# Kernel optimization log

Measured on AMD Instinct MI355X. Metric: run time of the kernel, lower is better.

The kernel has to match this reference:

```python
import jax, jax.numpy as jnp
import numpy as np
import math

G = 256        # graphs per batch
N = 2048       # nodes per graph (uniform)
D = 128        # dim_in
E = 4194304    # edges (avg degree 8)
DE = 16        # edge_attr dim
RATIO = 0.5    # cfg.gnn.pool_ratio


def setup_inputs() -> dict:
    key = jax.random.key(0)
    k1, k2, k3, k4 = jax.random.split(key, 4)
    x = jax.random.normal(k1, (G * N, D), jnp.float32)
    edge_index = jax.random.randint(k2, (2, E), 0, G * N, jnp.int32)
    edge_attr = jax.random.normal(k3, (E, DE), jnp.float32)
    batch = jnp.repeat(jnp.arange(G, dtype=jnp.int32), N)
    weight = jax.random.normal(k4, (D,), jnp.float32)  # TopKPooling score projection
    return {"x": x, "edge_index": edge_index, "edge_attr": edge_attr,
            "batch": batch, "weight": weight, "num_graphs": G}


def reference(x, edge_index, edge_attr, batch, weight, num_graphs):
    n_total = x.shape[0]
    n = n_total // num_graphs              # uniform nodes per graph
    k = int(math.ceil(RATIO * n))          # nodes kept per graph (static)

    # PyG TopKPooling score: tanh((x . w) / ||w||)
    score = jnp.tanh((x @ weight) / jnp.linalg.norm(weight))  # [n_total]

    # per-graph top-k (uniform graph sizes -> reshape + lax.top_k)
    top_idx = jax.lax.top_k(score.reshape(num_graphs, n), k)[1]          # [G, k]
    offs = (jnp.arange(num_graphs, dtype=top_idx.dtype) * n)[:, None]
    perm = (top_idx + offs).reshape(-1)                                  # [G*k] global node ids

    # gate kept node features by their score
    x_out = x[perm] * score[perm][:, None]                               # [G*k, D]
    batch_out = jnp.repeat(jnp.arange(num_graphs, dtype=batch.dtype), k)

    # filter_adj: remap kept nodes to new ids, drop edges touching removed nodes
    new_ids = jnp.arange(perm.shape[0], dtype=jnp.int32)
    node_map = jnp.full((n_total,), -1, jnp.int32).at[perm].set(new_ids)
    ns = node_map[edge_index[0]]
    nd = node_map[edge_index[1]]
    edge_mask = (ns >= 0) & (nd >= 0)                                    # [E]
    edge_index_out = jnp.where(edge_mask, jnp.stack([ns, nd]), -1)       # [2, E], -1 = dropped
    edge_attr_out = jnp.where(edge_mask[:, None], edge_attr, 0.0)        # [E, DE]

    return x_out, edge_index_out, edge_attr_out, batch_out, edge_mask
```

## Files before the change

kernel.cpp:

```cpp
#include <hip/hip_runtime.h>


__global__ void norm_kernel(const float* __restrict__ w,
                            float* __restrict__ inv_norm) {
  int l = threadIdx.x;
  float2 wv = reinterpret_cast<const float2*>(w)[l];
  float s = wv.x * wv.x + wv.y * wv.y;
#pragma unroll
  for (int off = 32; off > 0; off >>= 1) s += __shfl_xor(s, off);
  if (l == 0) *inv_norm = __frsqrt_rn(s);
}

__global__ __launch_bounds__(256) void score_kernel(
    const float* __restrict__ x, const float* __restrict__ w,
    const float* __restrict__ inv_norm, double* __restrict__ keys,
    float* __restrict__ gate, int n_total) {
  int t = (int)(blockIdx.x * 256u + threadIdx.x);
  int row = t >> 4;
  int sub = t & 15;
  if (row >= n_total) return;
  const float4* xp = reinterpret_cast<const float4*>(x + (size_t)row * 128 + sub * 8);
  const float4* wp = reinterpret_cast<const float4*>(w + sub * 8);
  float4 a = xp[0], b = xp[1];
  float4 wa = wp[0], wb = wp[1];
  double dot = (double)a.x * wa.x + (double)a.y * wa.y +
               (double)a.z * wa.z + (double)a.w * wa.w +
               (double)b.x * wb.x + (double)b.y * wb.y +
               (double)b.z * wb.z + (double)b.w * wb.w;
#pragma unroll
  for (int off = 8; off > 0; off >>= 1) dot += __shfl_xor(dot, off);
  if (sub == 0) {
    keys[row] = dot;
    gate[row] = tanhf((float)dot * inv_norm[0]);
  }
}

#define TK_PAD(j) ((j) + ((j) >> 4))
__global__ __launch_bounds__(1024) void topk_kernel(
    const double* __restrict__ keys, int* __restrict__ perm,
    int* __restrict__ node_map, int n, int k) {
  __shared__ unsigned long long skey[2048 + 128];
  __shared__ int sidx[2048 + 128];
  const int g = blockIdx.x;
  const int tid = threadIdx.x;

  for (int j = tid; j < n; j += 1024) {
    unsigned long long b =
        (unsigned long long)__double_as_longlong(keys[(size_t)g * n + j]);
    unsigned long long u = (b & 0x8000000000000000ULL) ? ~b : (b | 0x8000000000000000ULL);
    skey[TK_PAD(j)] = ~u;
    sidx[TK_PAD(j)] = j;
  }

  for (int size = 2; size <= n; size <<= 1) {
    for (int stride = size >> 1; stride > 0; stride >>= 1) {
      __syncthreads();
      int lo = ((tid & ~(stride - 1)) << 1) | (tid & (stride - 1));
      int hi = lo + stride;
      bool asc = ((lo & size) == 0);
      int plo = TK_PAD(lo), phi = TK_PAD(hi);
      unsigned long long ka = skey[plo], kb = skey[phi];
      int ia = sidx[plo], ib = sidx[phi];
      bool hi_lt_lo = (kb < ka) || (kb == ka && ib < ia);
      bool lo_lt_hi = (ka < kb) || (ka == kb && ia < ib);
      if (asc ? hi_lt_lo : lo_lt_hi) {
        skey[plo] = kb; skey[phi] = ka;
        sidx[plo] = ib; sidx[phi] = ia;
      }
    }
  }
  __syncthreads();

  for (int r = tid; r < n; r += 1024) {
    int node = g * n + sidx[TK_PAD(r)];
    node_map[node] = (r < k) ? (g * k + r) : -1;
    if (r < k) perm[g * k + r] = node;
  }
}

__global__ __launch_bounds__(256) void gather_kernel(
    const float* __restrict__ x, const float* __restrict__ gate,
    const int* __restrict__ perm, float* __restrict__ x_out,
    float* __restrict__ batch_out, int total_rows, int k) {
  int t = (int)(blockIdx.x * 256u + threadIdx.x);
  int row = t >> 5;
  int d4 = t & 31;
  if (row >= total_rows) return;
  int src = perm[row];
  float s = gate[src];
  float4 v = *reinterpret_cast<const float4*>(x + (size_t)src * 128 + d4 * 4);
  v.x *= s; v.y *= s; v.z *= s; v.w *= s;
  *reinterpret_cast<float4*>(x_out + (size_t)row * 128 + d4 * 4) = v;
  if (d4 == 0) batch_out[row] = (float)(row / k);
}

__global__ __launch_bounds__(256) void edge_kernel(
    const int* __restrict__ edge_index, const int* __restrict__ node_map,
    const float4* __restrict__ attr, float* __restrict__ eio,
    float* __restrict__ mask_out, float4* __restrict__ attr_out, int E) {
  __shared__ float smask[256];
  const int base = (int)(blockIdx.x * 256u);
  const int e = base + threadIdx.x;
  int ns = node_map[edge_index[e]];
  int nd = node_map[edge_index[E + e]];
  bool m = (ns >= 0) && (nd >= 0);
  float z = m ? 1.0f : 0.0f;
  eio[e] = m ? (float)ns : -1.0f;
  eio[E + e] = m ? (float)nd : -1.0f;
  mask_out[e] = z;
  smask[threadIdx.x] = z;
  __syncthreads();
  const float4* ablk = attr + (size_t)base * 4;
  float4* oblk = attr_out + (size_t)base * 4;
#pragma unroll
  for (int it = 0; it < 4; ++it) {
    int idx = it * 256 + (int)threadIdx.x;
    float zz = smask[idx >> 2];
    float4 a = ablk[idx];
    a.x *= zz; a.y *= zz; a.z *= zz; a.w *= zz;
    oblk[idx] = a;
  }
}

extern "C" void kernel_launch(void* const* d_in, const int* in_sizes, int n_in,
                              void* d_out, int out_size, void* d_ws, size_t ws_size,
                              hipStream_t stream) {
  const float* x          = (const float*)d_in[0];
  const int*   edge_index = (const int*)d_in[1];
  const float* edge_attr  = (const float*)d_in[2];
  const float* w          = (const float*)d_in[4];

  const int D = 128;
  const int n_total = in_sizes[0] / D;
  const int E = in_sizes[1] / 2;
  const int G = 256;
  const int n = n_total / G;
  const int k = (n + 1) / 2;
  const int total_rows = G * k;

  float* out       = (float*)d_out;
  float* x_out     = out;
  float* eio       = x_out + (size_t)total_rows * D;
  float* attr_out  = eio + (size_t)2 * E;
  float* batch_out = attr_out + (size_t)E * 16;
  float* mask_out  = batch_out + total_rows;

  double* keys   = (double*)d_ws;
  float* gate    = (float*)((char*)d_ws + (size_t)n_total * 8);
  int* perm      = (int*)(gate + n_total);
  int* node_map  = perm + total_rows;
  float* inv_nrm = (float*)(node_map + n_total);

  norm_kernel<<<1, 64, 0, stream>>>(w, inv_nrm);
  score_kernel<<<(n_total * 16) / 256, 256, 0, stream>>>(
      x, w, inv_nrm, keys, gate, n_total);
  topk_kernel<<<G, 1024, 0, stream>>>(keys, perm, node_map, n, k);
  gather_kernel<<<(total_rows * 32) / 256, 256, 0, stream>>>(
      x, gate, perm, x_out, batch_out, total_rows, k);
  edge_kernel<<<E / 256, 256, 0, stream>>>(
      edge_index, node_map, (const float4*)edge_attr, eio, mask_out,
      (float4*)attr_out, E);
}
```

Measured before the change: 272.3 us.

## Fuse gather and edge filter into one kernel, drop norm kernel, nontemporal stores

Merges the gather and edge-filter kernels into a single launch whose block index picks which of the two jobs a block does. The norm kernel and the stored gate array are removed: the gate tanh is recomputed in the gather path from the double keys, with the weight norm recomputed per block. Streaming loads and stores now use nontemporal builtins, and each block handles more rows or edges. This saves two launches and the gate traffic, at the cost of redundant per-block norm reductions and a branchy mixed-role kernel.

```diff
diff --git a/kernel.cpp b/kernel.cpp
--- a/kernel.cpp
+++ b/kernel.cpp
@@ -1,20 +1,20 @@
 #include <hip/hip_runtime.h>
 
 
-__global__ void norm_kernel(const float* __restrict__ w,
-                            float* __restrict__ inv_norm) {
-  int l = threadIdx.x;
-  float2 wv = reinterpret_cast<const float2*>(w)[l];
-  float s = wv.x * wv.x + wv.y * wv.y;
-#pragma unroll
-  for (int off = 32; off > 0; off >>= 1) s += __shfl_xor(s, off);
-  if (l == 0) *inv_norm = __frsqrt_rn(s);
+typedef float f32x4_v __attribute__((ext_vector_type(4)));
+
+__device__ inline void nt_store4(float4 v, float4* p) {
+  f32x4_v t; t.x = v.x; t.y = v.y; t.z = v.z; t.w = v.w;
+  __builtin_nontemporal_store(t, reinterpret_cast<f32x4_v*>(p));
+}
+__device__ inline float4 nt_load4(const float4* p) {
+  f32x4_v t = __builtin_nontemporal_load(reinterpret_cast<const f32x4_v*>(p));
+  return make_float4(t.x, t.y, t.z, t.w);
 }
 
 __global__ __launch_bounds__(256) void score_kernel(
     const float* __restrict__ x, const float* __restrict__ w,
-    const float* __restrict__ inv_norm, double* __restrict__ keys,
-    float* __restrict__ gate, int n_total) {
+    double* __restrict__ keys, int n_total) {
   int t = (int)(blockIdx.x * 256u + threadIdx.x);
   int row = t >> 4;
   int sub = t & 15;
@@ -29,10 +29,7 @@
                (double)b.z * wb.z + (double)b.w * wb.w;
 #pragma unroll
   for (int off = 8; off > 0; off >>= 1) dot += __shfl_xor(dot, off);
-  if (sub == 0) {
-    keys[row] = dot;
-    gate[row] = tanhf((float)dot * inv_norm[0]);
-  }
+  if (sub == 0) keys[row] = dot;
 }
 
 #define TK_PAD(j) ((j) + ((j) >> 4))
@@ -78,47 +75,64 @@
   }
 }
 
-__global__ __launch_bounds__(256) void gather_kernel(
-    const float* __restrict__ x, const float* __restrict__ gate,
-    const int* __restrict__ perm, float* __restrict__ x_out,
-    float* __restrict__ batch_out, int total_rows, int k) {
-  int t = (int)(blockIdx.x * 256u + threadIdx.x);
-  int row = t >> 5;
-  int d4 = t & 31;
-  if (row >= total_rows) return;
-  int src = perm[row];
-  float s = gate[src];
-  float4 v = *reinterpret_cast<const float4*>(x + (size_t)src * 128 + d4 * 4);
-  v.x *= s; v.y *= s; v.z *= s; v.w *= s;
-  *reinterpret_cast<float4*>(x_out + (size_t)row * 128 + d4 * 4) = v;
-  if (d4 == 0) batch_out[row] = (float)(row / k);
-}
+__global__ __launch_bounds__(256) void output_kernel(
+    const float* __restrict__ x, const double* __restrict__ keys,
+    const float* __restrict__ w, const int* __restrict__ perm,
+    const int* __restrict__ node_map, const int* __restrict__ edge_index,
+    const float4* __restrict__ attr, float* __restrict__ x_out,
+    float* __restrict__ batch_out, float* __restrict__ eio,
+    float* __restrict__ mask_out, float4* __restrict__ attr_out,
+    int E, int k, int NB_G) {
+  const int bid = (int)blockIdx.x;
+  if (bid < NB_G) {
+    int l = threadIdx.x & 63;
+    float2 wv = reinterpret_cast<const float2*>(w)[l];
+    float wsq = wv.x * wv.x + wv.y * wv.y;
+#pragma unroll
+    for (int off = 32; off > 0; off >>= 1) wsq += __shfl_xor(wsq, off);
+    float inv = __frsqrt_rn(wsq);
 
-__global__ __launch_bounds__(256) void edge_kernel(
-    const int* __restrict__ edge_index, const int* __restrict__ node_map,
-    const float4* __restrict__ attr, float* __restrict__ eio,
-    float* __restrict__ mask_out, float4* __restrict__ attr_out, int E) {
-  __shared__ float smask[256];
-  const int base = (int)(blockIdx.x * 256u);
-  const int e = base + threadIdx.x;
-  int ns = node_map[edge_index[e]];
-  int nd = node_map[edge_index[E + e]];
-  bool m = (ns >= 0) && (nd >= 0);
-  float z = m ? 1.0f : 0.0f;
-  eio[e] = m ? (float)ns : -1.0f;
-  eio[E + e] = m ? (float)nd : -1.0f;
-  mask_out[e] = z;
-  smask[threadIdx.x] = z;
-  __syncthreads();
-  const float4* ablk = attr + (size_t)base * 4;
-  float4* oblk = attr_out + (size_t)base * 4;
+    int d4 = threadIdx.x & 31;
+    int rbase = bid * 32 + ((int)threadIdx.x >> 5);
 #pragma unroll
-  for (int it = 0; it < 4; ++it) {
-    int idx = it * 256 + (int)threadIdx.x;
-    float zz = smask[idx >> 2];
-    float4 a = ablk[idx];
-    a.x *= zz; a.y *= zz; a.z *= zz; a.w *= zz;
-    oblk[idx] = a;
+    for (int r4 = 0; r4 < 4; ++r4) {
+      int row = rbase + r4 * 8;
+      int src = perm[row];
+      float s = tanhf((float)keys[src] * inv);
+      float4 v = *reinterpret_cast<const float4*>(x + (size_t)src * 128 + d4 * 4);
+      v.x *= s; v.y *= s; v.z *= s; v.w *= s;
+      nt_store4(v, reinterpret_cast<float4*>(x_out + (size_t)row * 128 + d4 * 4));
+      if (d4 == 0)
+        __builtin_nontemporal_store((float)(row / k), batch_out + row);
+    }
+  } else {
+    __shared__ float smask[256];
+    const int ebase = (bid - NB_G) * 512;
+    for (int it = 0; it < 2; ++it) {
+      int e = ebase + it * 256 + (int)threadIdx.x;
+      int s0 = __builtin_nontemporal_load(edge_index + e);
+      int s1 = __builtin_nontemporal_load(edge_index + E + e);
+      int ns = node_map[s0];
+      int nd = node_map[s1];
+      bool m = (ns >= 0) && (nd >= 0);
+      float z = m ? 1.0f : 0.0f;
+      __builtin_nontemporal_store(m ? (float)ns : -1.0f, eio + e);
+      __builtin_nontemporal_store(m ? (float)nd : -1.0f, eio + E + e);
+      __builtin_nontemporal_store(z, mask_out + e);
+      smask[threadIdx.x] = z;
+      __syncthreads();
+      const float4* ablk = attr + (size_t)(ebase + it * 256) * 4;
+      float4* oblk = attr_out + (size_t)(ebase + it * 256) * 4;
+#pragma unroll
+      for (int j = 0; j < 4; ++j) {
+        int idx = j * 256 + (int)threadIdx.x;
+        float zz = smask[idx >> 2];
+        float4 a = nt_load4(ablk + idx);
+        a.x *= zz; a.y *= zz; a.z *= zz; a.w *= zz;
+        nt_store4(a, oblk + idx);
+      }
+      __syncthreads();
+    }
   }
 }
 
@@ -145,19 +159,16 @@
   float* batch_out = attr_out + (size_t)E * 16;
   float* mask_out  = batch_out + total_rows;
 
-  double* keys   = (double*)d_ws;
-  float* gate    = (float*)((char*)d_ws + (size_t)n_total * 8);
-  int* perm      = (int*)(gate + n_total);
-  int* node_map  = perm + total_rows;
-  float* inv_nrm = (float*)(node_map + n_total);
+  double* keys  = (double*)d_ws;
+  int* perm     = (int*)((char*)d_ws + (size_t)n_total * 8);
+  int* node_map = perm + total_rows;
 
-  norm_kernel<<<1, 64, 0, stream>>>(w, inv_nrm);
-  score_kernel<<<(n_total * 16) / 256, 256, 0, stream>>>(
-      x, w, inv_nrm, keys, gate, n_total);
+  score_kernel<<<(n_total * 16) / 256, 256, 0, stream>>>(x, w, keys, n_total);
   topk_kernel<<<G, 1024, 0, stream>>>(keys, perm, node_map, n, k);
-  gather_kernel<<<(total_rows * 32) / 256, 256, 0, stream>>>(
-      x, gate, perm, x_out, batch_out, total_rows, k);
-  edge_kernel<<<E / 256, 256, 0, stream>>>(
-      edge_index, node_map, (const float4*)edge_attr, eio, mask_out,
-      (float4*)attr_out, E);
+
+  const int NB_G = total_rows / 32;
+  const int NB_E = E / 512;
+  output_kernel<<<NB_G + NB_E, 256, 0, stream>>>(
+      x, keys, w, perm, node_map, edge_index, (const float4*)edge_attr,
+      x_out, batch_out, eio, mask_out, (float4*)attr_out, E, k, NB_G);
 }
```

Measured after the change: 225.7 us. 1.21x faster.
